# Optimization experiments

Measured on AMD Instinct MI355X. Metric: run time of the kernel, lower is better.

## Reference

```python
import jax, jax.numpy as jnp
import numpy as np

N = 2048          # num nodes == in_channels (f1 = graphs[0].shape[0])
F_IN = 2048       # node feature dim
G1 = 10           # ChebConv out channels
E = 65536         # num edges (avg degree 32)
NUM_CLASSES = 10  # fc1 output


def setup_inputs() -> dict:
    key = jax.random.key(0)
    ks = jax.random.split(key, 6)
    x = jax.random.normal(ks[0], (N, F_IN), dtype=jnp.float32)
    edge_index = jax.random.randint(ks[1], (2, E), 0, N)
    # ChebConv weights: one [F_IN, G1] matrix per Chebyshev order (K=2), glorot-ish init
    s = float(1.0 / np.sqrt(F_IN))
    W0 = jax.random.uniform(ks[2], (F_IN, G1), jnp.float32, -s, s)
    W1 = jax.random.uniform(ks[3], (F_IN, G1), jnp.float32, -s, s)
    b = jnp.zeros((G1,), jnp.float32)
    sf = float(1.0 / np.sqrt(G1))
    Wf = jax.random.uniform(ks[4], (G1, NUM_CLASSES), jnp.float32, -sf, sf)
    bf = jax.random.uniform(ks[5], (NUM_CLASSES,), jnp.float32, -sf, sf)
    return {"x": x, "edge_index": edge_index, "W0": W0, "W1": W1, "b": b, "Wf": Wf, "bf": bf}


def _cheb_edge_weights(edge_index):
    # PyG ChebConv default: sym-normalized Laplacian scaled with lambda_max=2.0.
    # L_hat = 2*L/lambda_max - I = -D^{-1/2} A D^{-1/2}  (zero diagonal).
    row, col = edge_index[0], edge_index[1]
    deg = jax.ops.segment_sum(jnp.ones((E,), jnp.float32), row, num_segments=N)
    dis = jnp.where(deg > 0, jax.lax.rsqrt(jnp.maximum(deg, 1.0)), 0.0)
    return -dis[row] * dis[col]


def reference(x, edge_index, W0, W1, b, Wf, bf):
    row, col = edge_index[0], edge_index[1]
    w = _cheb_edge_weights(edge_index)
    # Tx_0 = x ; Tx_1 = L_hat @ x via gather (source=row) + scatter-add (target=col)
    Tx1 = jax.ops.segment_sum(w[:, None] * x[row], col, num_segments=N)  # [N, F_IN]
    h = x @ W0 + Tx1 @ W1 + b                                            # ChebConv, K=2
    h = jax.nn.relu(h)
    logits = h @ Wf + bf                                                 # fc1
    return jax.nn.log_softmax(logits, axis=1)
```

## Files before the change

kernel.cpp:

```cpp
#include <hip/hip_runtime.h>

#define N_NODES 2048
#define F_IN    2048
#define G1      10
#define NCLS    10
#define NEDGE   65536
#define JCHUNKS 32
#define JPER    64
#define HSLICES 128
#define ZSLICES 64

__device__ float g_p[JCHUNKS * 20 * N_NODES];
__device__ int   g_degp[HSLICES * N_NODES];
__device__ float g_dis[N_NODES];
__device__ float g_y[N_NODES * 20];
__device__ float g_zp[2 * ZSLICES * N_NODES * 5];

__global__ __launch_bounds__(256) void k_gemm(const float* __restrict__ x,
                                              const float* __restrict__ W0,
                                              const float* __restrict__ W1,
                                              const int* __restrict__ ei) {
    __shared__ float sx[256 * 33];
    int jc      = blockIdx.x;
    int rowbase = blockIdx.y * 256;

    float acc[20];
    #pragma unroll
    for (int k = 0; k < 20; ++k) acc[k] = 0.f;

    #pragma unroll
    for (int half = 0; half < 2; ++half) {
        int j0 = jc * JPER + half * 32;
        if (half) __syncthreads();
        #pragma unroll
        for (int rep = 0; rep < 8; ++rep) {
            int idx = rep * 256 + threadIdx.x;
            int r = idx >> 3, c4 = idx & 7;
            float4 v = *(const float4*)(x + (size_t)(rowbase + r) * F_IN + j0 + c4 * 4);
            float* d = sx + r * 33 + c4 * 4;
            d[0] = v.x; d[1] = v.y; d[2] = v.z; d[3] = v.w;
        }
        __syncthreads();
        const float* xr = sx + threadIdx.x * 33;
        #pragma unroll
        for (int j = 0; j < 32; ++j) {
            float xu = xr[j];
            const float* w0r = W0 + (size_t)(j0 + j) * G1;
            const float* w1r = W1 + (size_t)(j0 + j) * G1;
            #pragma unroll
            for (int k = 0; k < G1; ++k) {
                acc[k]      += xu * w0r[k];
                acc[10 + k] += xu * w1r[k];
            }
        }
    }
    int row = rowbase + threadIdx.x;
    #pragma unroll
    for (int k = 0; k < 20; ++k)
        g_p[((size_t)jc * 20 + k) * N_NODES + row] = acc[k];

    if (blockIdx.y < 4) {
        int slice = blockIdx.y * 32 + jc;
        __syncthreads();
        int* h = (int*)sx;
        for (int t = threadIdx.x; t < N_NODES; t += 256) h[t] = 0;
        __syncthreads();
        int base = slice * (NEDGE / HSLICES);
        #pragma unroll
        for (int u = 0; u < 2; ++u)
            atomicAdd(&h[ei[base + u * 256 + threadIdx.x]], 1);
        __syncthreads();
        for (int t = threadIdx.x; t < N_NODES; t += 256)
            g_degp[slice * N_NODES + t] = h[t];
    }
}

__global__ __launch_bounds__(256) void k_reduce() {
    int t   = blockIdx.x * 256 + threadIdx.x;
    int k   = t >> 11;
    int row = t & (N_NODES - 1);
    float s = 0.f;
    #pragma unroll 16
    for (int jc = 0; jc < JCHUNKS; ++jc)
        s += g_p[((size_t)jc * 20 + k) * N_NODES + row];
    g_y[row * 20 + k] = s;
    if (t < N_NODES) {
        int d = 0;
        #pragma unroll 16
        for (int sl = 0; sl < HSLICES; ++sl) d += g_degp[sl * N_NODES + t];
        g_dis[t] = (d > 0) ? rsqrtf((float)d) : 0.f;
    }
}

__global__ __launch_bounds__(256) void k_scatter(const int* __restrict__ ei) {
    __shared__ float zl[N_NODES * 5];
    int khalf  = blockIdx.x >> 6;
    int bslice = blockIdx.x & (ZSLICES - 1);
    float4* zl4 = (float4*)zl;
    #pragma unroll
    for (int t = threadIdx.x; t < N_NODES * 5 / 4; t += 256)
        zl4[t] = make_float4(0.f, 0.f, 0.f, 0.f);
    __syncthreads();
    int base = bslice * (NEDGE / ZSLICES);
    #pragma unroll
    for (int u = 0; u < NEDGE / ZSLICES / 256; ++u) {
        int e = base + u * 256 + threadIdx.x;
        int r = ei[e], c = ei[NEDGE + e];
        float w = -g_dis[r] * g_dis[c];
        const float* y1 = g_y + r * 20 + 10 + khalf * 5;
        float* zz = zl + c * 5;
        #pragma unroll
        for (int kk = 0; kk < 5; ++kk) atomicAdd(&zz[kk], w * y1[kk]);
    }
    __syncthreads();
    float4* dst = (float4*)(g_zp + ((size_t)khalf * ZSLICES + bslice) * (N_NODES * 5));
    #pragma unroll
    for (int t = threadIdx.x; t < N_NODES * 5 / 4; t += 256) dst[t] = zl4[t];
}

__global__ __launch_bounds__(256) void k_zf(const float* __restrict__ b,
                                            const float* __restrict__ Wf,
                                            const float* __restrict__ bfv,
                                            float* __restrict__ out) {
    __shared__ float zb[320];
    int nb = blockIdx.x * 32;
    for (int v = threadIdx.x; v < 320; v += 256) {
        int khalf = v / 160;
        int rem   = v - khalf * 160;
        int il    = rem / 5, kk = rem - il * 5;
        float s = 0.f;
        #pragma unroll 16
        for (int sl = 0; sl < ZSLICES; ++sl)
            s += g_zp[((size_t)khalf * ZSLICES + sl) * (N_NODES * 5) + (nb + il) * 5 + kk];
        zb[il * 10 + khalf * 5 + kk] = s;
    }
    __syncthreads();
    if (threadIdx.x < 32) {
        int i = nb + threadIdx.x;
        float h[G1];
        #pragma unroll
        for (int k = 0; k < G1; ++k)
            h[k] = fmaxf(g_y[i * 20 + k] + zb[threadIdx.x * 10 + k] + b[k], 0.f);
        float lo[NCLS];
        #pragma unroll
        for (int c = 0; c < NCLS; ++c) lo[c] = bfv[c];
        #pragma unroll
        for (int k = 0; k < G1; ++k) {
            float hk = h[k];
            #pragma unroll
            for (int c = 0; c < NCLS; ++c) lo[c] += hk * Wf[k * NCLS + c];
        }
        float m = lo[0];
        #pragma unroll
        for (int c = 1; c < NCLS; ++c) m = fmaxf(m, lo[c]);
        float s = 0.f;
        #pragma unroll
        for (int c = 0; c < NCLS; ++c) s += expf(lo[c] - m);
        float ls = logf(s);
        #pragma unroll
        for (int c = 0; c < NCLS; ++c) out[i * NCLS + c] = lo[c] - m - ls;
    }
}

extern "C" void kernel_launch(void* const* d_in, const int* in_sizes, int n_in,
                              void* d_out, int out_size, void* d_ws, size_t ws_size,
                              hipStream_t stream) {
    const float* x   = (const float*)d_in[0];
    const int*   ei  = (const int*)d_in[1];
    const float* W0  = (const float*)d_in[2];
    const float* W1  = (const float*)d_in[3];
    const float* b   = (const float*)d_in[4];
    const float* Wf  = (const float*)d_in[5];
    const float* bfv = (const float*)d_in[6];
    float* out = (float*)d_out;

    k_gemm<<<dim3(JCHUNKS, N_NODES / 256), 256, 0, stream>>>(x, W0, W1, ei);
    k_reduce<<<(N_NODES * 20) / 256, 256, 0, stream>>>();
    k_scatter<<<2 * ZSLICES, 256, 0, stream>>>(ei);
    k_zf<<<N_NODES / 32, 256, 0, stream>>>(b, Wf, bfv, out);
}
```

Before: 115.1 us.

## Split GEMM K-chunk across two thread halves with shared-memory reduction

The GEMM kernel now tiles 128 rows per block instead of 256 and loads the full 64-column x chunk in one pass. The two halves of the block each process 32 columns of that chunk for the same rows, then combine their partial sums through shared memory. This doubles the block count (512 vs 256) for better occupancy across CUs and removes the second load/sync phase, at the cost of an extra shared-memory reduction and barrier. The degree histogram slice mapping is adjusted to the new grid.

```diff
diff --git a/kernel.cpp b/kernel.cpp
--- a/kernel.cpp
+++ b/kernel.cpp
@@ -7,6 +7,7 @@
 #define NEDGE   65536
 #define JCHUNKS 32
 #define JPER    64
+#define RTILE   128
 #define HSLICES 128
 #define ZSLICES 64
 
@@ -20,58 +21,67 @@
                                               const float* __restrict__ W0,
                                               const float* __restrict__ W1,
                                               const int* __restrict__ ei) {
-    __shared__ float sx[256 * 33];
+    __shared__ float sx[RTILE * 65];
     int jc      = blockIdx.x;
-    int rowbase = blockIdx.y * 256;
+    int rowbase = blockIdx.y * RTILE;
+    int j0      = jc * JPER;
 
+    #pragma unroll
+    for (int rep = 0; rep < 8; ++rep) {
+        int idx = rep * 256 + threadIdx.x;
+        int r = idx >> 4, c4 = idx & 15;
+        float4 v = *(const float4*)(x + (size_t)(rowbase + r) * F_IN + j0 + c4 * 4);
+        float* d = sx + r * 65 + c4 * 4;
+        d[0] = v.x; d[1] = v.y; d[2] = v.z; d[3] = v.w;
+    }
+    __syncthreads();
+
+    int h = threadIdx.x >> 7;
+    int r = threadIdx.x & 127;
     float acc[20];
     #pragma unroll
     for (int k = 0; k < 20; ++k) acc[k] = 0.f;
 
+    const float* xr = sx + r * 65 + h * 32;
     #pragma unroll
-    for (int half = 0; half < 2; ++half) {
-        int j0 = jc * JPER + half * 32;
-        if (half) __syncthreads();
+    for (int j = 0; j < 32; ++j) {
+        float xu = xr[j];
+        int jcol = j0 + h * 32 + j;
+        const float* w0r = W0 + (size_t)jcol * G1;
+        const float* w1r = W1 + (size_t)jcol * G1;
         #pragma unroll
-        for (int rep = 0; rep < 8; ++rep) {
-            int idx = rep * 256 + threadIdx.x;
-            int r = idx >> 3, c4 = idx & 7;
-            float4 v = *(const float4*)(x + (size_t)(rowbase + r) * F_IN + j0 + c4 * 4);
-            float* d = sx + r * 33 + c4 * 4;
-            d[0] = v.x; d[1] = v.y; d[2] = v.z; d[3] = v.w;
-        }
-        __syncthreads();
-        const float* xr = sx + threadIdx.x * 33;
-        #pragma unroll
-        for (int j = 0; j < 32; ++j) {
-            float xu = xr[j];
-            const float* w0r = W0 + (size_t)(j0 + j) * G1;
-            const float* w1r = W1 + (size_t)(j0 + j) * G1;
-            #pragma unroll
-            for (int k = 0; k < G1; ++k) {
-                acc[k]      += xu * w0r[k];
-                acc[10 + k] += xu * w1r[k];
-            }
+        for (int k = 0; k < G1; ++k) {
+            acc[k]      += xu * w0r[k];
+            acc[10 + k] += xu * w1r[k];
         }
     }
-    int row = rowbase + threadIdx.x;
-    #pragma unroll
-    for (int k = 0; k < 20; ++k)
-        g_p[((size_t)jc * 20 + k) * N_NODES + row] = acc[k];
+    __syncthreads();
+    float* red = sx;
+    if (h == 1) {
+        #pragma unroll
+        for (int k = 0; k < 20; ++k) red[r * 21 + k] = acc[k];
+    }
+    __syncthreads();
+    if (h == 0) {
+        int row = rowbase + r;
+        #pragma unroll
+        for (int k = 0; k < 20; ++k)
+            g_p[((size_t)jc * 20 + k) * N_NODES + row] = acc[k] + red[r * 21 + k];
+    }
 
-    if (blockIdx.y < 4) {
-        int slice = blockIdx.y * 32 + jc;
+    if (blockIdx.y < 8 && jc < 16) {
+        int slice = blockIdx.y * 16 + jc;
         __syncthreads();
-        int* h = (int*)sx;
-        for (int t = threadIdx.x; t < N_NODES; t += 256) h[t] = 0;
+        int* hh = (int*)sx;
+        for (int t = threadIdx.x; t < N_NODES; t += 256) hh[t] = 0;
         __syncthreads();
         int base = slice * (NEDGE / HSLICES);
         #pragma unroll
         for (int u = 0; u < 2; ++u)
-            atomicAdd(&h[ei[base + u * 256 + threadIdx.x]], 1);
+            atomicAdd(&hh[ei[base + u * 256 + threadIdx.x]], 1);
         __syncthreads();
         for (int t = threadIdx.x; t < N_NODES; t += 256)
-            g_degp[slice * N_NODES + t] = h[t];
+            g_degp[slice * N_NODES + t] = hh[t];
     }
 }
 
@@ -174,7 +184,7 @@
     const float* bfv = (const float*)d_in[6];
     float* out = (float*)d_out;
 
-    k_gemm<<<dim3(JCHUNKS, N_NODES / 256), 256, 0, stream>>>(x, W0, W1, ei);
+    k_gemm<<<dim3(JCHUNKS, N_NODES / RTILE), 256, 0, stream>>>(x, W0, W1, ei);
     k_reduce<<<(N_NODES * 20) / 256, 256, 0, stream>>>();
     k_scatter<<<2 * ZSLICES, 256, 0, stream>>>(ei);
     k_zf<<<N_NODES / 32, 256, 0, stream>>>(b, Wf, bfv, out);
```

After: 112.7 us. 2.0% less time.
